# Performance work log

Measured on AMD Instinct MI355X. Metric: run time of the kernel, lower is better.

The kernel has to match this reference:

```python
import jax, jax.numpy as jnp
from jax import lax
import numpy as np

DECAY = 0.9
THRESH = 1.0


def setup_inputs() -> dict:
    key = jax.random.key(0)
    k1, k2, k3 = jax.random.split(key, 3)
    B, T, I, H, O = 64, 256, 1024, 2048, 1024
    x = jax.random.normal(k1, (B, T, I), dtype=jnp.float32)
    W1 = jax.random.normal(k2, (I, H), dtype=jnp.float32) * (1.0 / np.sqrt(I))
    b1 = jnp.zeros((H,), dtype=jnp.float32)
    W2 = jax.random.normal(k3, (H, O), dtype=jnp.float32) * (1.0 / np.sqrt(H))
    b2 = jnp.zeros((O,), dtype=jnp.float32)
    return {"x": x, "W1": W1, "b1": b1, "W2": W2, "b2": b2}


def reference(x, W1, b1, W2, b2):
    B, T, I = x.shape
    H = W1.shape[1]
    # Batch fc1 across all timesteps in one GEMM: [B,T,H]
    cur = jnp.einsum('bti,ih->bth', x, W1) + b1
    cur_tm = jnp.swapaxes(cur, 0, 1)  # [T,B,H] time-major for scan

    def step(carry, cur_t):
        mem, _ = carry
        mem = mem * DECAY + cur_t * (1.0 - DECAY)
        fired = mem > THRESH
        spk = jnp.where(fired, 1.0, 0.0).astype(mem.dtype)
        mem = jnp.where(fired, 0.0, mem)
        return (mem, spk), None

    mem0 = jnp.zeros((B, H), dtype=x.dtype)
    spk0 = jnp.zeros((B, H), dtype=x.dtype)
    (_, spk_last), _ = lax.scan(step, (mem0, spk0), cur_tm)
    # fc2 applied only to the final spike pattern, as in the original
    return spk_last @ W2 + b2
```

## Files before the change

kernel.cpp:

```cpp
#include <hip/hip_runtime.h>


typedef __attribute__((ext_vector_type(16))) float f32x16;
typedef __attribute__((ext_vector_type(8))) short s16x8;

#define GPTR(p) ((const __attribute__((address_space(1))) void*)(p))
#define SPTR(p) ((__attribute__((address_space(3))) void*)(p))

static constexpr int Bsz = 64, Tsz = 256, Isz = 1024, Hsz = 2048, Osz = 1024;
static constexpr int BK = 32;
static constexpr int NKT = Isz / BK;
static constexpr int AH_OFF = 0, AL_OFF = 8192, BH_OFF = 16384, BL_OFF = 24576;
static constexpr int BUFEL = 32768;
static constexpr int SCAN_STRIDE = 260;
static constexpr int LDS_USHORTS = 128 * SCAN_STRIDE * 2;

__device__ __forceinline__ unsigned short f2bf(float f) {
  unsigned u = __float_as_uint(f);
  u += 0x7FFFu + ((u >> 16) & 1u);
  return (unsigned short)(u >> 16);
}
__device__ __forceinline__ float bf2f(unsigned short h) {
  return __uint_as_float(((unsigned)h) << 16);
}

__global__ void split_x_kernel(const float* __restrict__ x,
                               unsigned short* __restrict__ hi,
                               unsigned short* __restrict__ lo) {
  const long i = (long)blockIdx.x * 256 + threadIdx.x;
  const float4 v = ((const float4*)x)[i];
  const unsigned short hx = f2bf(v.x), hy = f2bf(v.y), hz = f2bf(v.z), hw = f2bf(v.w);
  ushort4 H, L;
  H.x = hx; H.y = hy; H.z = hz; H.w = hw;
  L.x = f2bf(v.x - bf2f(hx));
  L.y = f2bf(v.y - bf2f(hy));
  L.z = f2bf(v.z - bf2f(hz));
  L.w = f2bf(v.w - bf2f(hw));
  ((ushort4*)hi)[i] = H;
  ((ushort4*)lo)[i] = L;
}

__global__ void w1_transpose_split_kernel(const float* __restrict__ W1,
                                          unsigned short* __restrict__ wh,
                                          unsigned short* __restrict__ wl) {
  __shared__ float tile[32][33];
  const int h0 = blockIdx.x * 32;
  const int i0 = blockIdx.y * 32;
  const int c = threadIdx.x & 31;
  const int r4 = threadIdx.x >> 5;
#pragma unroll
  for (int s = 0; s < 4; ++s) {
    const int r = r4 + s * 8;
    tile[r][c] = W1[(long)(i0 + r) * Hsz + h0 + c];
  }
  __syncthreads();
#pragma unroll
  for (int s = 0; s < 4; ++s) {
    const int hr = r4 + s * 8;
    const float v = tile[c][hr];
    const unsigned short hh = f2bf(v);
    wh[(long)(h0 + hr) * Isz + i0 + c] = hh;
    wl[(long)(h0 + hr) * Isz + i0 + c] = f2bf(v - bf2f(hh));
  }
}

__global__ __launch_bounds__(256, 1) void gemm1_scan_kernel(
    const unsigned short* __restrict__ xh, const unsigned short* __restrict__ xl,
    const unsigned short* __restrict__ wth, const unsigned short* __restrict__ wtl,
    const float* __restrict__ b1, float* __restrict__ spk) {
  __shared__ __align__(16) unsigned short lds[LDS_USHORTS];

  const int tid = threadIdx.x;
  const int l = tid & 63;
  const int w = tid >> 6;
  const int wm = w >> 1;
  const int wn = w & 1;
  const int b = blockIdx.y;
  const int hb = blockIdx.x * 256;

  const int srow = tid >> 2;
  const int gch8 = ((tid & 3) ^ ((tid >> 3) & 3)) * 8;
  const unsigned short* gAh = xh + (long)(b * Tsz + srow) * Isz + gch8;
  const unsigned short* gAl = xl + (long)(b * Tsz + srow) * Isz + gch8;
  const unsigned short* gBh = wth + (long)(hb + srow) * Isz + gch8;
  const unsigned short* gBl = wtl + (long)(hb + srow) * Isz + gch8;

#define STG(OFF, G, KT) do {                                                              \
    unsigned short* d_ = lds + ((KT) & 1) * BUFEL + (OFF) + tid * 8;                      \
    __builtin_amdgcn_global_load_lds(GPTR((G) + (long)(KT) * BK), SPTR(d_), 16, 0, 0);    \
    __builtin_amdgcn_global_load_lds(GPTR((G) + 64 * Isz + (long)(KT) * BK), SPTR(d_ + 2048), 16, 0, 0); \
    __builtin_amdgcn_global_load_lds(GPTR((G) + 128 * Isz + (long)(KT) * BK), SPTR(d_ + 4096), 16, 0, 0); \
    __builtin_amdgcn_global_load_lds(GPTR((G) + 192 * Isz + (long)(KT) * BK), SPTR(d_ + 6144), 16, 0, 0); \
  } while (0)

  const int lr = l & 31;
  const int swzf = (l >> 1) & 3;
  const int chK0 = (((l >> 5)) ^ swzf) * 8;
  const int chK1 = ((2 + (l >> 5)) ^ swzf) * 8;
  const int abase = (wm * 128 + lr) * 32;
  const int bbase = (wn * 128 + lr) * 32;

  f32x16 acc[4][4];
#pragma unroll
  for (int i = 0; i < 4; ++i)
#pragma unroll
    for (int j = 0; j < 4; ++j) acc[i][j] = (f32x16)(0.f);

#define MM(MI, NI, AF, BF) \
  acc[MI][NI] = __builtin_amdgcn_mfma_f32_32x32x16_bf16(AF, BF, acc[MI][NI], 0, 0, 0)

#define BAR() __builtin_amdgcn_s_barrier()
#define SBAR() __builtin_amdgcn_sched_barrier(0)
#define WAITLGKM(N) do { asm volatile("s_waitcnt lgkmcnt(" #N ")" ::: "memory"); SBAR(); } while (0)

  STG(AH_OFF, gAh, 0);
  STG(BH_OFF, gBh, 0);
  STG(AL_OFF, gAl, 0);
  STG(BL_OFF, gBl, 0);
  asm volatile("s_waitcnt vmcnt(8)" ::: "memory");
  BAR();

  s16x8 Ah0[4], Ah1[4], Al0[4], Al1[4], Bh0[4], Bh1[4], Bl0[4], Bl1[4];

  for (int kt = 0; kt < NKT; ++kt) {
    const unsigned short* p = lds + (kt & 1) * BUFEL;
    const bool st = (kt + 1) < NKT;

#pragma unroll
    for (int mi = 0; mi < 4; ++mi) Ah0[mi] = *(const s16x8*)(p + AH_OFF + abase + mi * 1024 + chK0);
#pragma unroll
    for (int ni = 0; ni < 4; ++ni) Bh0[ni] = *(const s16x8*)(p + BH_OFF + bbase + ni * 1024 + chK0);
    SBAR();
#pragma unroll
    for (int mi = 0; mi < 4; ++mi) Ah1[mi] = *(const s16x8*)(p + AH_OFF + abase + mi * 1024 + chK1);
#pragma unroll
    for (int ni = 0; ni < 4; ++ni) Bh1[ni] = *(const s16x8*)(p + BH_OFF + bbase + ni * 1024 + chK1);
    if (st) { STG(AH_OFF, gAh, kt + 1); STG(BH_OFF, gBh, kt + 1); }
    WAITLGKM(8);
    __builtin_amdgcn_s_setprio(1);
#pragma unroll
    for (int mi = 0; mi < 4; ++mi)
#pragma unroll
      for (int ni = 0; ni < 4; ++ni) MM(mi, ni, Ah0[mi], Bh0[ni]);
    WAITLGKM(0);
#pragma unroll
    for (int mi = 0; mi < 4; ++mi)
#pragma unroll
      for (int ni = 0; ni < 4; ++ni) MM(mi, ni, Ah1[mi], Bh1[ni]);
    __builtin_amdgcn_s_setprio(0);
    if (st) asm volatile("s_waitcnt vmcnt(8)" ::: "memory");
    else    asm volatile("s_waitcnt vmcnt(0)" ::: "memory");
    BAR();

#pragma unroll
    for (int ni = 0; ni < 4; ++ni) {
      Bl0[ni] = *(const s16x8*)(p + BL_OFF + bbase + ni * 1024 + chK0);
      Bl1[ni] = *(const s16x8*)(p + BL_OFF + bbase + ni * 1024 + chK1);
    }
    SBAR();
#pragma unroll
    for (int mi = 0; mi < 4; ++mi) {
      Al0[mi] = *(const s16x8*)(p + AL_OFF + abase + mi * 1024 + chK0);
      Al1[mi] = *(const s16x8*)(p + AL_OFF + abase + mi * 1024 + chK1);
    }
    if (st) { STG(AL_OFF, gAl, kt + 1); STG(BL_OFF, gBl, kt + 1); }
    WAITLGKM(8);
    __builtin_amdgcn_s_setprio(1);
#pragma unroll
    for (int mi = 0; mi < 4; ++mi)
#pragma unroll
      for (int ni = 0; ni < 4; ++ni) MM(mi, ni, Ah0[mi], Bl0[ni]);
#pragma unroll
    for (int mi = 0; mi < 4; ++mi)
#pragma unroll
      for (int ni = 0; ni < 4; ++ni) MM(mi, ni, Ah1[mi], Bl1[ni]);
    WAITLGKM(0);
#pragma unroll
    for (int mi = 0; mi < 4; ++mi)
#pragma unroll
      for (int ni = 0; ni < 4; ++ni) MM(mi, ni, Al0[mi], Bh0[ni]);
#pragma unroll
    for (int mi = 0; mi < 4; ++mi)
#pragma unroll
      for (int ni = 0; ni < 4; ++ni) MM(mi, ni, Al1[mi], Bh1[ni]);
    __builtin_amdgcn_s_setprio(0);
    asm volatile("s_waitcnt vmcnt(8)" ::: "memory");
    BAR();
  }

  __syncthreads();
  float* scanbuf = reinterpret_cast<float*>(lds);
  float memv = 0.f;
  int fired = 0;
  const float b1v = b1[hb + tid];

  for (int rnd = 0; rnd < 2; ++rnd) {
    if (wm == rnd) {
#pragma unroll
      for (int mi = 0; mi < 4; ++mi)
#pragma unroll
        for (int ni = 0; ni < 4; ++ni) {
          const int col = wn * 128 + ni * 32 + lr;
#pragma unroll
          for (int r = 0; r < 16; ++r) {
            const int trow = mi * 32 + (r & 3) + 8 * (r >> 2) + 4 * (l >> 5);
            scanbuf[trow * SCAN_STRIDE + col] = acc[mi][ni][r];
          }
        }
    }
    __syncthreads();
    {
      for (int t = 0; t < 128; ++t) {
        const float c = scanbuf[t * SCAN_STRIDE + tid] + b1v;
        memv = memv * 0.9f + c * 0.1f;
        fired = memv > 1.0f;
        if (fired) memv = 0.f;
      }
    }
    __syncthreads();
  }
  spk[(long)b * Hsz + hb + tid] = fired ? 1.0f : 0.0f;
}

__global__ void gemm2_kernel(const float* __restrict__ spk, const float* __restrict__ W2,
                             const float* __restrict__ b2, float* __restrict__ out) {
  __shared__ int s_cnt[256];
  __shared__ int s_off[257];
  __shared__ int s_list[Hsz];
  const int b = blockIdx.x;
  const int tid = threadIdx.x;
  int hs[8];
  int c = 0;
#pragma unroll
  for (int e = 0; e < 8; ++e) {
    const int h = tid * 8 + e;
    if (spk[(long)b * Hsz + h] > 0.5f) hs[c++] = h;
  }
  s_cnt[tid] = c;
  __syncthreads();
  if (tid == 0) {
    int s = 0;
    for (int i = 0; i < 256; ++i) { s_off[i] = s; s += s_cnt[i]; }
    s_off[256] = s;
  }
  __syncthreads();
  {
    const int base = s_off[tid];
    for (int i = 0; i < c; ++i) s_list[base + i] = hs[i];
  }
  __syncthreads();
  const int total = s_off[256];
#pragma unroll
  for (int q = 0; q < 4; ++q) {
    const int o = q * 256 + tid;
    float v = b2[o];
    for (int i = 0; i < total; ++i) v += W2[(long)s_list[i] * Osz + o];
    out[(long)b * Osz + o] = v;
  }
}

extern "C" void kernel_launch(void* const* d_in, const int* in_sizes, int n_in,
                              void* d_out, int out_size, void* d_ws, size_t ws_size,
                              hipStream_t stream) {
  const float* x = (const float*)d_in[0];
  const float* W1 = (const float*)d_in[1];
  const float* b1 = (const float*)d_in[2];
  const float* W2 = (const float*)d_in[3];
  const float* b2 = (const float*)d_in[4];
  float* out = (float*)d_out;

  unsigned short* xh = (unsigned short*)d_ws;
  unsigned short* xl = xh + (long)Bsz * Tsz * Isz;
  unsigned short* wh = xl + (long)Bsz * Tsz * Isz;
  unsigned short* wl = wh + (long)Hsz * Isz;
  float* spk = (float*)(wl + (long)Hsz * Isz);

  split_x_kernel<<<(Bsz * Tsz * Isz) / (256 * 4), 256, 0, stream>>>(x, xh, xl);
  w1_transpose_split_kernel<<<dim3(Hsz / 32, Isz / 32), 256, 0, stream>>>(W1, wh, wl);
  gemm1_scan_kernel<<<dim3(8, 64), 256, 0, stream>>>(xh, xl, wh, wl, b1, spk);
  gemm2_kernel<<<Bsz, 256, 0, stream>>>(spk, W2, b2, out);
}
```

Measured before the change: 209.0 us.

## Issue all next-tile loads at once, drop mid-iteration barrier, transpose scan buffer

The GEMM main loop now issues all four global-to-LDS stages for the next K tile together and removes the mid-iteration barrier and vmcnt wait. It also interleaves the B-low fragment reads with the second hi*hi MFMA batch, leaving one barrier per K step with a full vmcnt(0) drain. The scan buffer changes from time-major to hidden-major with stride 132, so each thread stores accumulator quads as float4 and the scan reads four timesteps per vector load, prefetching the next quad. The aim is fewer synchronisations and fewer LDS instructions, at the cost of a full memory drain each iteration, which may expose load latency.

```diff
diff --git a/kernel.cpp b/kernel.cpp
--- a/kernel.cpp
+++ b/kernel.cpp
@@ -12,8 +12,8 @@
 static constexpr int NKT = Isz / BK;
 static constexpr int AH_OFF = 0, AL_OFF = 8192, BH_OFF = 16384, BL_OFF = 24576;
 static constexpr int BUFEL = 32768;
-static constexpr int SCAN_STRIDE = 260;
-static constexpr int LDS_USHORTS = 128 * SCAN_STRIDE * 2;
+static constexpr int ST = 132;
+static constexpr int LDS_USHORTS = 256 * ST * 2;
 
 __device__ __forceinline__ unsigned short f2bf(float f) {
   unsigned u = __float_as_uint(f);
@@ -117,7 +117,7 @@
   STG(BH_OFF, gBh, 0);
   STG(AL_OFF, gAl, 0);
   STG(BL_OFF, gBl, 0);
-  asm volatile("s_waitcnt vmcnt(8)" ::: "memory");
+  asm volatile("s_waitcnt vmcnt(0)" ::: "memory");
   BAR();
 
   s16x8 Ah0[4], Ah1[4], Al0[4], Al1[4], Bh0[4], Bh1[4], Bl0[4], Bl1[4];
@@ -135,37 +135,34 @@
     for (int mi = 0; mi < 4; ++mi) Ah1[mi] = *(const s16x8*)(p + AH_OFF + abase + mi * 1024 + chK1);
 #pragma unroll
     for (int ni = 0; ni < 4; ++ni) Bh1[ni] = *(const s16x8*)(p + BH_OFF + bbase + ni * 1024 + chK1);
-    if (st) { STG(AH_OFF, gAh, kt + 1); STG(BH_OFF, gBh, kt + 1); }
+    SBAR();
+    if (st) { STG(AH_OFF, gAh, kt + 1); STG(BH_OFF, gBh, kt + 1);
+              STG(AL_OFF, gAl, kt + 1); STG(BL_OFF, gBl, kt + 1); }
+    SBAR();
     WAITLGKM(8);
     __builtin_amdgcn_s_setprio(1);
 #pragma unroll
     for (int mi = 0; mi < 4; ++mi)
 #pragma unroll
       for (int ni = 0; ni < 4; ++ni) MM(mi, ni, Ah0[mi], Bh0[ni]);
-    WAITLGKM(0);
-#pragma unroll
-    for (int mi = 0; mi < 4; ++mi)
-#pragma unroll
-      for (int ni = 0; ni < 4; ++ni) MM(mi, ni, Ah1[mi], Bh1[ni]);
-    __builtin_amdgcn_s_setprio(0);
-    if (st) asm volatile("s_waitcnt vmcnt(8)" ::: "memory");
-    else    asm volatile("s_waitcnt vmcnt(0)" ::: "memory");
-    BAR();
-
+    SBAR();
 #pragma unroll
     for (int ni = 0; ni < 4; ++ni) {
       Bl0[ni] = *(const s16x8*)(p + BL_OFF + bbase + ni * 1024 + chK0);
       Bl1[ni] = *(const s16x8*)(p + BL_OFF + bbase + ni * 1024 + chK1);
     }
+    WAITLGKM(8);
+#pragma unroll
+    for (int mi = 0; mi < 4; ++mi)
+#pragma unroll
+      for (int ni = 0; ni < 4; ++ni) MM(mi, ni, Ah1[mi], Bh1[ni]);
     SBAR();
 #pragma unroll
     for (int mi = 0; mi < 4; ++mi) {
       Al0[mi] = *(const s16x8*)(p + AL_OFF + abase + mi * 1024 + chK0);
       Al1[mi] = *(const s16x8*)(p + AL_OFF + abase + mi * 1024 + chK1);
     }
-    if (st) { STG(AL_OFF, gAl, kt + 1); STG(BL_OFF, gBl, kt + 1); }
     WAITLGKM(8);
-    __builtin_amdgcn_s_setprio(1);
 #pragma unroll
     for (int mi = 0; mi < 4; ++mi)
 #pragma unroll
@@ -184,7 +181,7 @@
 #pragma unroll
       for (int ni = 0; ni < 4; ++ni) MM(mi, ni, Al1[mi], Bh1[ni]);
     __builtin_amdgcn_s_setprio(0);
-    asm volatile("s_waitcnt vmcnt(8)" ::: "memory");
+    asm volatile("s_waitcnt vmcnt(0)" ::: "memory");
     BAR();
   }
 
@@ -201,20 +198,31 @@
 #pragma unroll
         for (int ni = 0; ni < 4; ++ni) {
           const int col = wn * 128 + ni * 32 + lr;
-#pragma unroll
-          for (int r = 0; r < 16; ++r) {
-            const int trow = mi * 32 + (r & 3) + 8 * (r >> 2) + 4 * (l >> 5);
-            scanbuf[trow * SCAN_STRIDE + col] = acc[mi][ni][r];
+          float* dst = scanbuf + col * ST + mi * 32 + 4 * (l >> 5);
+#pragma unroll
+          for (int rq = 0; rq < 4; ++rq) {
+            float4 v;
+            v.x = acc[mi][ni][rq * 4 + 0];
+            v.y = acc[mi][ni][rq * 4 + 1];
+            v.z = acc[mi][ni][rq * 4 + 2];
+            v.w = acc[mi][ni][rq * 4 + 3];
+            *reinterpret_cast<float4*>(dst + 8 * rq) = v;
           }
         }
     }
     __syncthreads();
     {
-      for (int t = 0; t < 128; ++t) {
-        const float c = scanbuf[t * SCAN_STRIDE + tid] + b1v;
-        memv = memv * 0.9f + c * 0.1f;
-        fired = memv > 1.0f;
-        if (fired) memv = 0.f;
+      const float* src = scanbuf + tid * ST;
+      float4 cur = *reinterpret_cast<const float4*>(src);
+      for (int t0 = 0; t0 < 128; t0 += 4) {
+        const int tn = (t0 + 4 < 128) ? t0 + 4 : t0;
+        const float4 nxt = *reinterpret_cast<const float4*>(src + tn);
+        float c;
+        c = cur.x + b1v; memv = memv * 0.9f + c * 0.1f; fired = memv > 1.0f; if (fired) memv = 0.f;
+        c = cur.y + b1v; memv = memv * 0.9f + c * 0.1f; fired = memv > 1.0f; if (fired) memv = 0.f;
+        c = cur.z + b1v; memv = memv * 0.9f + c * 0.1f; fired = memv > 1.0f; if (fired) memv = 0.f;
+        c = cur.w + b1v; memv = memv * 0.9f + c * 0.1f; fired = memv > 1.0f; if (fired) memv = 0.f;
+        cur = nxt;
       }
     }
     __syncthreads();
```

After: 210.5 us. Within noise of the previous version (+0.7%).
